# Kernel optimization log

Hardware: AMD Instinct MI355X
Metric: run time of the kernel (lower is better)

## Reference

```python
import jax, jax.numpy as jnp
from jax import lax
import numpy as np

H = 768          # BERT-base hidden size
NLAB = 2         # labelnum
T = NLAB + 2     # CRF tagset incl START/STOP (NCRF++ convention)
START = NLAB     # index 2
STOP = NLAB + 1  # index 3


def setup_inputs() -> dict:
    key = jax.random.key(0)
    ks = jax.random.split(key, 8)
    B, S1 = 64, 513  # S1 = 1 (CLS) + 512 content tokens
    emb = jax.random.normal(ks[0], (B, S1, H), dtype=jnp.float32)
    answer_seq_label = jax.random.randint(ks[1], (B, S1), 0, NLAB)
    IsQA = jax.random.randint(ks[2], (B,), 0, 2)
    fc2_W = jax.random.normal(ks[3], (2, H), dtype=jnp.float32) * 0.02
    fc2_b = jnp.zeros((2,), dtype=jnp.float32)
    crf_W = jax.random.normal(ks[4], (T, H), dtype=jnp.float32) * 0.02
    crf_b = jnp.zeros((T,), dtype=jnp.float32)
    transitions = jax.random.normal(ks[5], (T, T), dtype=jnp.float32) * 0.1
    return {"emb": emb, "answer_seq_label": answer_seq_label, "IsQA": IsQA,
            "fc2_W": fc2_W, "fc2_b": fc2_b, "crf_W": crf_W, "crf_b": crf_b,
            "transitions": transitions}


def _crf_log_partition(feats, trans):
    # feats [B,S,T]; linear-chain forward algorithm (log-sum-exp scan)
    alpha0 = feats[:, 0] + trans[START][None]           # [B,T]
    def step(alpha, feat_t):
        # alpha[b,prev] + trans[prev,cur] -> logsumexp over prev
        new = jax.nn.logsumexp(alpha[:, :, None] + trans[None], axis=1) + feat_t
        return new, None
    alpha, _ = lax.scan(step, alpha0, jnp.swapaxes(feats[:, 1:], 0, 1))
    return jax.nn.logsumexp(alpha + trans[:, STOP][None], axis=1)  # [B]


def _crf_gold_score(feats, tags, trans):
    # feats [B,S,T], tags [B,S]
    emit = jnp.take_along_axis(feats, tags[:, :, None], axis=2)[..., 0].sum(axis=1)
    tr = trans[tags[:, :-1], tags[:, 1:]].sum(axis=1)
    tr = tr + trans[START, tags[:, 0]] + trans[tags[:, -1], STOP]
    return emit + tr


def _crf_viterbi(feats, trans):
    # feats [B,S,T] -> best path [B,S]
    delta0 = feats[:, 0] + trans[START][None]
    def step(delta, feat_t):
        scores = delta[:, :, None] + trans[None]   # [B,prev,cur]
        bp = jnp.argmax(scores, axis=1)            # [B,T]
        return jnp.max(scores, axis=1) + feat_t, bp
    delta, bps = lax.scan(step, delta0, jnp.swapaxes(feats[:, 1:], 0, 1))  # bps [S-1,B,T]
    last_tag = jnp.argmax(delta + trans[:, STOP][None], axis=1)            # [B]
    def back(tag, bp_t):
        prev = jnp.take_along_axis(bp_t, tag[:, None], axis=1)[:, 0]
        return prev, prev
    _, path_prefix = lax.scan(back, last_tag, bps, reverse=True)           # [S-1,B]
    return jnp.concatenate([path_prefix, last_tag[None]], axis=0).T        # [B,S]


def reference(emb, answer_seq_label, IsQA, fc2_W, fc2_b, crf_W, crf_b, transitions):
    # CLS head + cross-entropy
    cls_emb = emb[:, 0]                              # [B,H]
    isqa_logits = cls_emb @ fc2_W.T + fc2_b          # [B,2]
    logp = jax.nn.log_softmax(isqa_logits, axis=-1)
    isqa_loss = -jnp.take_along_axis(logp, IsQA[:, None], axis=1).mean()
    isqa_pred = jnp.argmax(isqa_logits, axis=-1)[:, None]
    # CRF head (dropout = identity in eval); feats [B,S,T]
    feats = jnp.einsum('bsh,th->bst', emb[:, 1:], crf_W) + crf_b
    tags = answer_seq_label[:, 1:]
    Z = _crf_log_partition(feats, transitions)
    gold = _crf_gold_score(feats, tags, transitions)
    crf_loss = jnp.mean(Z - gold)
    crf_pred = _crf_viterbi(feats, transitions)
    return (isqa_pred, crf_pred, isqa_loss, crf_loss, tags, IsQA[:, None])
```

## Files before the change

### kernel.cpp

```cpp
#include <hip/hip_runtime.h>
#include <math.h>

#define B     64
#define S1    513
#define S     512
#define H     768
#define T     4
#define START 2
#define STOP  3

#define OUT_ISQA_PRED 0
#define OUT_CRF_PRED  64
#define OUT_ISQA_LOSS 32832
#define OUT_CRF_LOSS  32833
#define OUT_TAGS      32834
#define OUT_ISQA      65602

#define WS_FEATS  0
#define WS_LOGITS (B*S*T)
#define WS_ZG     (B*S*T + 2*B)
#define WS_CNT    (B*S*T + 3*B)
#define WS_FEATST 131280

template<int CTRL>
__device__ __forceinline__ float dppf(float x) {
    int v = __builtin_amdgcn_update_dpp(__builtin_bit_cast(int, x),
                                        __builtin_bit_cast(int, x),
                                        CTRL, 0xF, 0xF, false);
    return __builtin_bit_cast(float, v);
}
template<int CTRL>
__device__ __forceinline__ int dppi(int x) {
    return __builtin_amdgcn_update_dpp(x, x, CTRL, 0xF, 0xF, false);
}

__device__ __forceinline__ float lse4(float x0, float x1, float x2, float x3) {
    float m = fmaxf(fmaxf(x0, x1), fmaxf(x2, x3));
    return m + __logf(__expf(x0 - m) + __expf(x1 - m) +
                      __expf(x2 - m) + __expf(x3 - m));
}

__device__ __forceinline__ float wred(float a) {
    a += dppf<0xB1>(a); a += dppf<0x4E>(a);
    a += __shfl_xor(a, 4); a += __shfl_xor(a, 8);
    a += __shfl_xor(a, 16); a += __shfl_xor(a, 32);
    return a;
}

__global__ __launch_bounds__(256) void feats_kernel(
    const float* __restrict__ emb,
    const float* __restrict__ crf_W, const float* __restrict__ crf_b,
    float* __restrict__ ws)
{
    if (blockIdx.x == 0 && threadIdx.x == 0)
        ((int*)ws)[WS_CNT] = 0;

    const int tid  = threadIdx.x;
    const int lane = tid & 63;
    const int wid  = blockIdx.x * 4 + (tid >> 6);

    const float4* __restrict__ W4 = (const float4*)crf_W;
    float4 wr[4][3];
    #pragma unroll
    for (int o = 0; o < 4; ++o)
        #pragma unroll
        for (int k = 0; k < 3; ++k)
            wr[o][k] = W4[o * 192 + lane + 64 * k];
    const float cb0 = crf_b[0], cb1 = crf_b[1], cb2 = crf_b[2], cb3 = crf_b[3];

    float* __restrict__ fN = ws + WS_FEATS;
    float* __restrict__ fT = ws + WS_FEATST;

    #pragma unroll
    for (int i = 0; i < 8; ++i) {
        const int row = wid + 4096 * i;
        const int b   = row >> 9;
        const int s   = (row & 511) + 1;
        const float4* __restrict__ src4 =
            (const float4*)emb + (size_t)(b * S1 + s) * (H / 4);

        float a0 = 0.f, a1 = 0.f, a2 = 0.f, a3 = 0.f;
        #pragma unroll
        for (int k = 0; k < 3; ++k) {
            const float4 e = src4[lane + 64 * k];
            a0 += e.x * wr[0][k].x + e.y * wr[0][k].y + e.z * wr[0][k].z + e.w * wr[0][k].w;
            a1 += e.x * wr[1][k].x + e.y * wr[1][k].y + e.z * wr[1][k].z + e.w * wr[1][k].w;
            a2 += e.x * wr[2][k].x + e.y * wr[2][k].y + e.z * wr[2][k].z + e.w * wr[2][k].w;
            a3 += e.x * wr[3][k].x + e.y * wr[3][k].y + e.z * wr[3][k].z + e.w * wr[3][k].w;
        }
        a0 = wred(a0); a1 = wred(a1); a2 = wred(a2); a3 = wred(a3);

        if (lane == 0) {
            const float v0 = a0 + cb0, v1 = a1 + cb1, v2 = a2 + cb2, v3 = a3 + cb3;
            ((float4*)fN)[b * S + (s - 1)] = make_float4(v0, v1, v2, v3);
            const int tb = b * 4 * S + (s - 1);
            fT[tb + 0 * S] = v0;
            fT[tb + 1 * S] = v1;
            fT[tb + 2 * S] = v2;
            fT[tb + 3 * S] = v3;
        }
    }
}

__device__ __forceinline__ unsigned int vstep(
    float& d, float fv,
    float tc0, float tc1, float tc2, float tc3, int sh8j)
{
    const float d0 = dppf<0x00>(d), d1 = dppf<0x55>(d);
    const float d2 = dppf<0xAA>(d), d3 = dppf<0xFF>(d);
    const float y0 = d0 + tc0, y1 = d1 + tc1;
    const float y2 = d2 + tc2, y3 = d3 + tc3;
    const float m01 = fmaxf(y0, y1), m23 = fmaxf(y2, y3);
    const int   i01 = (y1 > y0) ? 1 : 0;
    const int   i23 = (y3 > y2) ? 3 : 2;
    const int   bi  = (m23 > m01) ? i23 : i01;
    d = fmaxf(m01, m23) + fv;
    unsigned int mb = (unsigned int)bi << sh8j;
    unsigned int t1 = mb | (unsigned int)dppi<0xB1>((int)mb);
    return t1 | (unsigned int)dppi<0x4E>((int)t1);
}

__global__ __launch_bounds__(256) void crf_kernel(
    const int* __restrict__ ans, const int* __restrict__ isqa,
    const float* __restrict__ emb,
    const float* __restrict__ fc2_W, const float* __restrict__ fc2_b,
    const float* __restrict__ trans,
    float* __restrict__ ws, float* __restrict__ out)
{
    __shared__ float smemf[10784];
    __shared__ int isLast;
    const int tid = threadIdx.x;
    const int blk = blockIdx.x;

    if (blk < 64) {
        const int b = blk;
        float* sf  = smemf;
        float* C   = smemf + 2048;
        float* red = smemf + 3072;

        float tr[16];
        #pragma unroll
        for (int i = 0; i < 16; ++i) tr[i] = trans[i];

        {
            float4* sf4 = (float4*)sf;
            const float4* src4 = (const float4*)(ws + WS_FEATS) + b * 512;
            sf4[tid] = src4[tid];
            sf4[tid + 256] = src4[tid + 256];
        }

        if (tid < 128) {
            const int wv   = tid >> 6;
            const int lane = tid & 63;
            const float4* e4 = (const float4*)emb + (size_t)b * S1 * (H / 4);
            const float4* w4 = (const float4*)fc2_W + wv * 192;
            float acc = 0.f;
            #pragma unroll
            for (int k = 0; k < 3; ++k) {
                const float4 e = e4[lane + 64 * k];
                const float4 w = w4[lane + 64 * k];
                acc += e.x * w.x + e.y * w.y + e.z * w.z + e.w * w.w;
            }
            acc = wred(acc);
            if (lane == 0) {
                ws[WS_LOGITS + 2 * b + wv] = acc + fc2_b[wv];
                __threadfence();
            }
        }
        __syncthreads();

        float g = 0.f;
        #pragma unroll
        for (int u = 0; u < 2; ++u) {
            const int t   = 2 * tid + u;
            const int tag = ans[b * S1 + 1 + t];
            out[OUT_TAGS + b * S + t] = (float)tag;
            g += sf[t * 4 + tag];
            g += (t == 0) ? tr[START * 4 + tag] : tr[ans[b * S1 + t] * 4 + tag];
            if (t == S - 1) g += tr[tag * 4 + STOP];
        }
        #pragma unroll
        for (int m = 32; m; m >>= 1) g += __shfl_xor(g, m);
        if ((tid & 63) == 0) red[tid >> 6] = g;

        const int c  = tid >> 2;
        const int jr = tid & 3;
        const int t0 = c ? 8 * c : 1;
        float rl[4];
        #pragma unroll
        for (int i = 0; i < 4; ++i) rl[i] = tr[jr * 4 + i] + sf[t0 * 4 + i];
        for (int t = t0 + 1; t <= 8 * c + 7; ++t) {
            const float f0 = sf[t*4+0], f1 = sf[t*4+1], f2 = sf[t*4+2], f3 = sf[t*4+3];
            float nr[4];
            #pragma unroll
            for (int i = 0; i < 4; ++i)
                nr[i] = lse4(rl[0] + tr[0*4+i], rl[1] + tr[1*4+i],
                             rl[2] + tr[2*4+i], rl[3] + tr[3*4+i]);
            rl[0] = nr[0] + f0; rl[1] = nr[1] + f1;
            rl[2] = nr[2] + f2; rl[3] = nr[3] + f3;
        }
        ((float4*)C)[c * 4 + jr] = make_float4(rl[0], rl[1], rl[2], rl[3]);
        __syncthreads();

        for (int d = 1; d <= 32; d <<= 1) {
            const int cs = (c >= d) ? (c - d) : c;
            float4 ar = ((float4*)C)[cs * 4 + jr];
            float4 b0 = ((float4*)C)[c * 4 + 0];
            float4 b1 = ((float4*)C)[c * 4 + 1];
            float4 b2 = ((float4*)C)[c * 4 + 2];
            float4 b3 = ((float4*)C)[c * 4 + 3];
            __syncthreads();
            if (c >= d) {
                float4 nr;
                nr.x = lse4(ar.x + b0.x, ar.y + b1.x, ar.z + b2.x, ar.w + b3.x);
                nr.y = lse4(ar.x + b0.y, ar.y + b1.y, ar.z + b2.y, ar.w + b3.y);
                nr.z = lse4(ar.x + b0.z, ar.y + b1.z, ar.z + b2.z, ar.w + b3.z);
                nr.w = lse4(ar.x + b0.w, ar.y + b1.w, ar.z + b2.w, ar.w + b3.w);
                ((float4*)C)[c * 4 + jr] = nr;
            }
            __syncthreads();
        }

        if (tid == 0) {
            const float gold = red[0] + red[1] + red[2] + red[3];
            float a0k[4];
            #pragma unroll
            for (int k = 0; k < 4; ++k) a0k[k] = sf[k] + tr[START * 4 + k];
            const float* P = C + 63 * 16;
            float aN[4];
            #pragma unroll
            for (int i = 0; i < 4; ++i)
                aN[i] = lse4(a0k[0] + P[0*4+i], a0k[1] + P[1*4+i],
                             a0k[2] + P[2*4+i], a0k[3] + P[3*4+i]);
            const float Z = lse4(aN[0] + tr[0*4+STOP], aN[1] + tr[1*4+STOP],
                                 aN[2] + tr[2*4+STOP], aN[3] + tr[3*4+STOP]);
            ws[WS_ZG + b] = Z - gold;
            out[OUT_ISQA + b] = (float)isqa[b];
            __threadfence();
            const int old = atomicAdd((int*)ws + WS_CNT, 1);
            isLast = (old == 63);
        }
        __syncthreads();

        if (isLast && tid < 64) {
            __threadfence();
            const float zg = ws[WS_ZG + tid];
            const float l0 = ws[WS_LOGITS + tid * 2 + 0];
            const float l1 = ws[WS_LOGITS + tid * 2 + 1];
            const float m  = fmaxf(l0, l1);
            const float lse = m + __logf(__expf(l0 - m) + __expf(l1 - m));
            const int   y   = isqa[tid];
            const float li  = lse - (y ? l1 : l0);
            float s1 = zg, s2 = li;
            #pragma unroll
            for (int d = 32; d; d >>= 1) {
                s1 += __shfl_xor(s1, d);
                s2 += __shfl_xor(s2, d);
            }
            out[OUT_ISQA_PRED + tid] = (l1 > l0) ? 1.0f : 0.0f;
            if (tid == 0) {
                out[OUT_CRF_LOSS]  = s1 * (1.0f / 64.0f);
                out[OUT_ISQA_LOSS] = s2 * (1.0f / 64.0f);
            }
        }
    } else {
        const int bv = blk - 64;
        float* sfT = smemf;
        unsigned int* bpw = (unsigned int*)(smemf + 8208);
        {
            float4* d4 = (float4*)sfT;
            const float4* s4 = (const float4*)(ws + WS_FEATST) + bv * 4 * 512;
            #pragma unroll
            for (int n = 0; n < 8; ++n) d4[tid + 256 * n] = s4[tid + 256 * n];
        }
        if (tid < 4) ((float4*)(sfT + 8192))[tid & 3] =
            make_float4(0.f, 0.f, 0.f, 0.f);
        __syncthreads();

        const int w    = tid >> 6;
        const int lane = tid & 63;
        const int j    = lane & 3;
        const int b    = bv * 4 + w;
        const int sh8j = 8 * j;

        const float tc0 = trans[0*4+j], tc1 = trans[1*4+j];
        const float tc2 = trans[2*4+j], tc3 = trans[3*4+j];
        const float tSj = trans[START*4+j];
        const float tjs = trans[j*4 + STOP];

        const float4* colT4 = (const float4*)(sfT + w * 2048 + j * 512);
        uint4* bpq = (uint4*)(bpw + w * 512);

        float4 A  = colT4[0];
        float4 Bq = colT4[1];
        float4 B2 = colT4[2];
        float d = A.x + tSj;
        {
            const unsigned int W1 = vstep(d, A.y, tc0, tc1, tc2, tc3, sh8j);
            const unsigned int W2 = vstep(d, A.z, tc0, tc1, tc2, tc3, sh8j);
            const unsigned int W3 = vstep(d, A.w, tc0, tc1, tc2, tc3, sh8j);
            if (lane == 0) bpq[0] = make_uint4(0x03020100u, W1, W2, W3);
        }
        for (int g = 1; g < 128; ++g) {
            const float4 Cq = colT4[g + 2];
            const unsigned int W0 = vstep(d, Bq.x, tc0, tc1, tc2, tc3, sh8j);
            const unsigned int W1 = vstep(d, Bq.y, tc0, tc1, tc2, tc3, sh8j);
            const unsigned int W2 = vstep(d, Bq.z, tc0, tc1, tc2, tc3, sh8j);
            const unsigned int W3 = vstep(d, Bq.w, tc0, tc1, tc2, tc3, sh8j);
            if (lane == 0) bpq[g] = make_uint4(W0, W1, W2, W3);
            Bq = B2; B2 = Cq;
        }

        const float vj = d + tjs;
        const float z0 = dppf<0x00>(vj), z1 = dppf<0x55>(vj);
        const float z2 = dppf<0xAA>(vj), z3 = dppf<0xFF>(vj);
        float m01 = z0; unsigned int i01 = 0;
        if (z1 > m01) { m01 = z1; i01 = 1; }
        float m23 = z2; unsigned int i23 = 2;
        if (z3 > m23) { m23 = z3; i23 = 3; }
        const unsigned int lt = (m23 > m01) ? i23 : i01;

        __syncthreads();

        const uint4 wv0 = bpq[lane * 2 + 0];
        const uint4 wv1 = bpq[lane * 2 + 1];
        unsigned int wk[8] = {wv0.x, wv0.y, wv0.z, wv0.w, wv1.x, wv1.y, wv1.z, wv1.w};
        unsigned int G = wk[7];
        #pragma unroll
        for (int k = 6; k >= 0; --k)
            G = __builtin_amdgcn_perm(0u, wk[k], G);
        unsigned int Sm = G;
        #pragma unroll
        for (int dd = 1; dd < 64; dd <<= 1) {
            const int srcl = lane + dd;
            const unsigned int oth = __shfl(Sm, (srcl < 64) ? srcl : 63);
            if (srcl < 64) Sm = __builtin_amdgcn_perm(0u, Sm, oth);
        }
        unsigned int emap = __shfl(Sm, (lane < 63) ? lane + 1 : 63);
        if (lane == 63) emap = 0x03020100u;
        unsigned int cur = (emap >> (8 * lt)) & 3u;

        float tg[8];
        tg[7] = (float)cur;
        #pragma unroll
        for (int k = 7; k >= 1; --k) {
            cur = (wk[k] >> (8 * cur)) & 3u;
            tg[k - 1] = (float)cur;
        }
        float4* op = (float4*)(out + OUT_CRF_PRED + b * S + lane * 8);
        op[0] = make_float4(tg[0], tg[1], tg[2], tg[3]);
        op[1] = make_float4(tg[4], tg[5], tg[6], tg[7]);
    }
}

extern "C" void kernel_launch(void* const* d_in, const int* in_sizes, int n_in,
                              void* d_out, int out_size, void* d_ws, size_t ws_size,
                              hipStream_t stream)
{
    const float* emb    = (const float*)d_in[0];
    const int*   ans    = (const int*)d_in[1];
    const int*   isqa   = (const int*)d_in[2];
    const float* fc2_W  = (const float*)d_in[3];
    const float* fc2_b  = (const float*)d_in[4];
    const float* crf_W  = (const float*)d_in[5];
    const float* crf_b  = (const float*)d_in[6];
    const float* trans  = (const float*)d_in[7];
    float* out = (float*)d_out;
    float* ws  = (float*)d_ws;

    feats_kernel<<<1024, 256, 0, stream>>>(emb, crf_W, crf_b, ws);
    crf_kernel<<<80, 256, 0, stream>>>(ans, isqa, emb, fc2_W, fc2_b, trans, ws, out);
}
```

Baseline: 195.1 us.

## Fuse feats and CRF kernels into one cooperative launch with grid sync

Merges the emission-feature projection and the CRF/Viterbi stage into a single cooperative kernel of 512 blocks separated by a grid-wide sync, removing one launch and the gap between kernels. Each wave now handles two rows per iteration so more loads are in flight. Viterbi backpointers are kept in per-lane registers through predicated selects instead of going through shared memory and a block barrier. Costs are a grid sync, fewer blocks for the memory-bound projection, and extra register pressure and compare work in the Viterbi loop.

```diff
diff --git a/kernel.cpp b/kernel.cpp
--- a/kernel.cpp
+++ b/kernel.cpp
@@ -1,5 +1,8 @@
 #include <hip/hip_runtime.h>
+#include <hip/hip_cooperative_groups.h>
 #include <math.h>
+
+namespace cg = cooperative_groups;
 
 #define B     64
 #define S1    513
@@ -47,59 +50,8 @@
     return a;
 }
 
-__global__ __launch_bounds__(256) void feats_kernel(
-    const float* __restrict__ emb,
-    const float* __restrict__ crf_W, const float* __restrict__ crf_b,
-    float* __restrict__ ws)
-{
-    if (blockIdx.x == 0 && threadIdx.x == 0)
-        ((int*)ws)[WS_CNT] = 0;
-
-    const int tid  = threadIdx.x;
-    const int lane = tid & 63;
-    const int wid  = blockIdx.x * 4 + (tid >> 6);
-
-    const float4* __restrict__ W4 = (const float4*)crf_W;
-    float4 wr[4][3];
-    #pragma unroll
-    for (int o = 0; o < 4; ++o)
-        #pragma unroll
-        for (int k = 0; k < 3; ++k)
-            wr[o][k] = W4[o * 192 + lane + 64 * k];
-    const float cb0 = crf_b[0], cb1 = crf_b[1], cb2 = crf_b[2], cb3 = crf_b[3];
-
-    float* __restrict__ fN = ws + WS_FEATS;
-    float* __restrict__ fT = ws + WS_FEATST;
-
-    #pragma unroll
-    for (int i = 0; i < 8; ++i) {
-        const int row = wid + 4096 * i;
-        const int b   = row >> 9;
-        const int s   = (row & 511) + 1;
-        const float4* __restrict__ src4 =
-            (const float4*)emb + (size_t)(b * S1 + s) * (H / 4);
-
-        float a0 = 0.f, a1 = 0.f, a2 = 0.f, a3 = 0.f;
-        #pragma unroll
-        for (int k = 0; k < 3; ++k) {
-            const float4 e = src4[lane + 64 * k];
-            a0 += e.x * wr[0][k].x + e.y * wr[0][k].y + e.z * wr[0][k].z + e.w * wr[0][k].w;
-            a1 += e.x * wr[1][k].x + e.y * wr[1][k].y + e.z * wr[1][k].z + e.w * wr[1][k].w;
-            a2 += e.x * wr[2][k].x + e.y * wr[2][k].y + e.z * wr[2][k].z + e.w * wr[2][k].w;
-            a3 += e.x * wr[3][k].x + e.y * wr[3][k].y + e.z * wr[3][k].z + e.w * wr[3][k].w;
-        }
-        a0 = wred(a0); a1 = wred(a1); a2 = wred(a2); a3 = wred(a3);
-
-        if (lane == 0) {
-            const float v0 = a0 + cb0, v1 = a1 + cb1, v2 = a2 + cb2, v3 = a3 + cb3;
-            ((float4*)fN)[b * S + (s - 1)] = make_float4(v0, v1, v2, v3);
-            const int tb = b * 4 * S + (s - 1);
-            fT[tb + 0 * S] = v0;
-            fT[tb + 1 * S] = v1;
-            fT[tb + 2 * S] = v2;
-            fT[tb + 3 * S] = v3;
-        }
-    }
+__device__ __forceinline__ float dot4(float4 e, float4 w) {
+    return e.x * w.x + e.y * w.y + e.z * w.z + e.w * w.w;
 }
 
 __device__ __forceinline__ unsigned int vstep(
@@ -120,17 +72,81 @@
     return t1 | (unsigned int)dppi<0x4E>((int)t1);
 }
 
-__global__ __launch_bounds__(256) void crf_kernel(
+__global__ __launch_bounds__(256) void fused_kernel(
     const int* __restrict__ ans, const int* __restrict__ isqa,
     const float* __restrict__ emb,
     const float* __restrict__ fc2_W, const float* __restrict__ fc2_b,
+    const float* __restrict__ crf_W, const float* __restrict__ crf_b,
     const float* __restrict__ trans,
     float* __restrict__ ws, float* __restrict__ out)
 {
-    __shared__ float smemf[10784];
+    __shared__ float smemf[8208];
     __shared__ int isLast;
-    const int tid = threadIdx.x;
-    const int blk = blockIdx.x;
+    const int tid  = threadIdx.x;
+    const int lane = tid & 63;
+    const int blk  = blockIdx.x;
+
+    if (blk == 0 && tid == 0) ((int*)ws)[WS_CNT] = 0;
+    {
+        const int wid = blk * 4 + (tid >> 6);
+        const float4* __restrict__ W4 = (const float4*)crf_W;
+        float4 wr[4][3];
+        #pragma unroll
+        for (int o = 0; o < 4; ++o)
+            #pragma unroll
+            for (int k = 0; k < 3; ++k)
+                wr[o][k] = W4[o * 192 + lane + 64 * k];
+        const float cb0 = crf_b[0], cb1 = crf_b[1], cb2 = crf_b[2], cb3 = crf_b[3];
+        float* __restrict__ fN = ws + WS_FEATS;
+        float* __restrict__ fT = ws + WS_FEATST;
+
+        #pragma unroll 2
+        for (int i = 0; i < 16; i += 2) {
+            const int r0 = wid + 2048 * i;
+            const int r1 = wid + 2048 * (i + 1);
+            const int b0 = r0 >> 9, s0 = (r0 & 511) + 1;
+            const int b1 = r1 >> 9, s1 = (r1 & 511) + 1;
+            const float4* __restrict__ p0 =
+                (const float4*)emb + (size_t)(b0 * S1 + s0) * (H / 4);
+            const float4* __restrict__ p1 =
+                (const float4*)emb + (size_t)(b1 * S1 + s1) * (H / 4);
+            float4 e0[3], e1[3];
+            #pragma unroll
+            for (int k = 0; k < 3; ++k) e0[k] = p0[lane + 64 * k];
+            #pragma unroll
+            for (int k = 0; k < 3; ++k) e1[k] = p1[lane + 64 * k];
+
+            float a00 = 0.f, a01 = 0.f, a02 = 0.f, a03 = 0.f;
+            float a10 = 0.f, a11 = 0.f, a12 = 0.f, a13 = 0.f;
+            #pragma unroll
+            for (int k = 0; k < 3; ++k) {
+                a00 += dot4(e0[k], wr[0][k]); a01 += dot4(e0[k], wr[1][k]);
+                a02 += dot4(e0[k], wr[2][k]); a03 += dot4(e0[k], wr[3][k]);
+                a10 += dot4(e1[k], wr[0][k]); a11 += dot4(e1[k], wr[1][k]);
+                a12 += dot4(e1[k], wr[2][k]); a13 += dot4(e1[k], wr[3][k]);
+            }
+            a00 = wred(a00); a01 = wred(a01); a02 = wred(a02); a03 = wred(a03);
+            a10 = wred(a10); a11 = wred(a11); a12 = wred(a12); a13 = wred(a13);
+
+            if (lane == 0) {
+                const float v0 = a00 + cb0, v1 = a01 + cb1;
+                const float v2 = a02 + cb2, v3 = a03 + cb3;
+                ((float4*)fN)[b0 * S + (s0 - 1)] = make_float4(v0, v1, v2, v3);
+                const int tb0 = b0 * 4 * S + (s0 - 1);
+                fT[tb0 + 0 * S] = v0; fT[tb0 + 1 * S] = v1;
+                fT[tb0 + 2 * S] = v2; fT[tb0 + 3 * S] = v3;
+                const float u0 = a10 + cb0, u1 = a11 + cb1;
+                const float u2 = a12 + cb2, u3 = a13 + cb3;
+                ((float4*)fN)[b1 * S + (s1 - 1)] = make_float4(u0, u1, u2, u3);
+                const int tb1 = b1 * 4 * S + (s1 - 1);
+                fT[tb1 + 0 * S] = u0; fT[tb1 + 1 * S] = u1;
+                fT[tb1 + 2 * S] = u2; fT[tb1 + 3 * S] = u3;
+            }
+        }
+    }
+
+    __threadfence();
+    cg::this_grid().sync();
 
     if (blk < 64) {
         const int b = blk;
@@ -150,8 +166,7 @@
         }
 
         if (tid < 128) {
-            const int wv   = tid >> 6;
-            const int lane = tid & 63;
+            const int wv = tid >> 6;
             const float4* e4 = (const float4*)emb + (size_t)b * S1 * (H / 4);
             const float4* w4 = (const float4*)fc2_W + wv * 192;
             float acc = 0.f;
@@ -159,7 +174,7 @@
             for (int k = 0; k < 3; ++k) {
                 const float4 e = e4[lane + 64 * k];
                 const float4 w = w4[lane + 64 * k];
-                acc += e.x * w.x + e.y * w.y + e.z * w.z + e.w * w.w;
+                acc += dot4(e, w);
             }
             acc = wred(acc);
             if (lane == 0) {
@@ -263,10 +278,9 @@
                 out[OUT_ISQA_LOSS] = s2 * (1.0f / 64.0f);
             }
         }
-    } else {
+    } else if (blk < 80) {
         const int bv = blk - 64;
         float* sfT = smemf;
-        unsigned int* bpw = (unsigned int*)(smemf + 8208);
         {
             float4* d4 = (float4*)sfT;
             const float4* s4 = (const float4*)(ws + WS_FEATST) + bv * 4 * 512;
@@ -278,7 +292,6 @@
         __syncthreads();
 
         const int w    = tid >> 6;
-        const int lane = tid & 63;
         const int j    = lane & 3;
         const int b    = bv * 4 + w;
         const int sh8j = 8 * j;
@@ -289,8 +302,8 @@
         const float tjs = trans[j*4 + STOP];
 
         const float4* colT4 = (const float4*)(sfT + w * 2048 + j * 512);
-        uint4* bpq = (uint4*)(bpw + w * 512);
-
+
+        unsigned int wk[8] = {0, 0, 0, 0, 0, 0, 0, 0};
         float4 A  = colT4[0];
         float4 Bq = colT4[1];
         float4 B2 = colT4[2];
@@ -299,7 +312,7 @@
             const unsigned int W1 = vstep(d, A.y, tc0, tc1, tc2, tc3, sh8j);
             const unsigned int W2 = vstep(d, A.z, tc0, tc1, tc2, tc3, sh8j);
             const unsigned int W3 = vstep(d, A.w, tc0, tc1, tc2, tc3, sh8j);
-            if (lane == 0) bpq[0] = make_uint4(0x03020100u, W1, W2, W3);
+            if (lane == 0) { wk[0] = 0x03020100u; wk[1] = W1; wk[2] = W2; wk[3] = W3; }
         }
         for (int g = 1; g < 128; ++g) {
             const float4 Cq = colT4[g + 2];
@@ -307,7 +320,8 @@
             const unsigned int W1 = vstep(d, Bq.y, tc0, tc1, tc2, tc3, sh8j);
             const unsigned int W2 = vstep(d, Bq.z, tc0, tc1, tc2, tc3, sh8j);
             const unsigned int W3 = vstep(d, Bq.w, tc0, tc1, tc2, tc3, sh8j);
-            if (lane == 0) bpq[g] = make_uint4(W0, W1, W2, W3);
+            if (g == 2 * lane)     { wk[0] = W0; wk[1] = W1; wk[2] = W2; wk[3] = W3; }
+            if (g == 2 * lane + 1) { wk[4] = W0; wk[5] = W1; wk[6] = W2; wk[7] = W3; }
             Bq = B2; B2 = Cq;
         }
 
@@ -320,11 +334,6 @@
         if (z3 > m23) { m23 = z3; i23 = 3; }
         const unsigned int lt = (m23 > m01) ? i23 : i01;
 
-        __syncthreads();
-
-        const uint4 wv0 = bpq[lane * 2 + 0];
-        const uint4 wv1 = bpq[lane * 2 + 1];
-        unsigned int wk[8] = {wv0.x, wv0.y, wv0.z, wv0.w, wv1.x, wv1.y, wv1.z, wv1.w};
         unsigned int G = wk[7];
         #pragma unroll
         for (int k = 6; k >= 0; --k)
@@ -357,9 +366,9 @@
                               void* d_out, int out_size, void* d_ws, size_t ws_size,
                               hipStream_t stream)
 {
-    const float* emb    = (const float*)d_in[0];
     const int*   ans    = (const int*)d_in[1];
     const int*   isqa   = (const int*)d_in[2];
+    const float* emb    = (const float*)d_in[0];
     const float* fc2_W  = (const float*)d_in[3];
     const float* fc2_b  = (const float*)d_in[4];
     const float* crf_W  = (const float*)d_in[5];
@@ -368,6 +377,9 @@
     float* out = (float*)d_out;
     float* ws  = (float*)d_ws;
 
-    feats_kernel<<<1024, 256, 0, stream>>>(emb, crf_W, crf_b, ws);
-    crf_kernel<<<80, 256, 0, stream>>>(ans, isqa, emb, fc2_W, fc2_b, trans, ws, out);
-}
+    void* args[] = {(void*)&ans, (void*)&isqa, (void*)&emb,
+                    (void*)&fc2_W, (void*)&fc2_b, (void*)&crf_W, (void*)&crf_b,
+                    (void*)&trans, (void*)&ws, (void*)&out};
+    hipLaunchCooperativeKernel((void*)fused_kernel, dim3(512), dim3(256),
+                               args, 0, stream);
+}
```

New measurement: 312.0 us. 59.9% more time.

## Compute CRF emission feats with one thread per row instead of one wave per row

Applied to the files above, without the earlier changes.

The feats kernel now assigns each token row to a single thread that loops over the full hidden dimension, reading emb and the broadcast crf_W directly. This removes the cross-lane wave reductions and the 8-row loop per wave, and the launch shrinks to 512 blocks of 64 threads. In exchange, lanes in a wave read rows spaced 3 KB apart, so the loads are no longer coalesced. The kernel also runs far fewer waves, which reduces latency hiding on a bandwidth-bound read.

```diff
diff --git a/kernel.cpp b/kernel.cpp
--- a/kernel.cpp
+++ b/kernel.cpp
@@ -47,7 +47,11 @@
     return a;
 }
 
-__global__ __launch_bounds__(256) void feats_kernel(
+__device__ __forceinline__ float dot4(float4 e, float4 w) {
+    return e.x * w.x + e.y * w.y + e.z * w.z + e.w * w.w;
+}
+
+__global__ __launch_bounds__(64) void feats_kernel(
     const float* __restrict__ emb,
     const float* __restrict__ crf_W, const float* __restrict__ crf_b,
     float* __restrict__ ws)
@@ -55,51 +59,42 @@
     if (blockIdx.x == 0 && threadIdx.x == 0)
         ((int*)ws)[WS_CNT] = 0;
 
-    const int tid  = threadIdx.x;
-    const int lane = tid & 63;
-    const int wid  = blockIdx.x * 4 + (tid >> 6);
-
+    const int lane = threadIdx.x;
+    const int r    = blockIdx.x * 64 + lane;
+    const int b    = r >> 9;
+    const int s    = (r & 511) + 1;
+
+    const float4* __restrict__ src4 =
+        (const float4*)emb + (size_t)(b * S1 + s) * (H / 4);
     const float4* __restrict__ W4 = (const float4*)crf_W;
-    float4 wr[4][3];
-    #pragma unroll
-    for (int o = 0; o < 4; ++o)
-        #pragma unroll
-        for (int k = 0; k < 3; ++k)
-            wr[o][k] = W4[o * 192 + lane + 64 * k];
-    const float cb0 = crf_b[0], cb1 = crf_b[1], cb2 = crf_b[2], cb3 = crf_b[3];
+
+    float a0 = 0.f, a1 = 0.f, a2 = 0.f, a3 = 0.f;
+    #pragma unroll 8
+    for (int k = 0; k < 192; ++k) {
+        const float4 e  = src4[k];
+        const float4 w0 = W4[0 * 192 + k];
+        const float4 w1 = W4[1 * 192 + k];
+        const float4 w2 = W4[2 * 192 + k];
+        const float4 w3 = W4[3 * 192 + k];
+        a0 += dot4(e, w0);
+        a1 += dot4(e, w1);
+        a2 += dot4(e, w2);
+        a3 += dot4(e, w3);
+    }
+
+    const float v0 = a0 + crf_b[0];
+    const float v1 = a1 + crf_b[1];
+    const float v2 = a2 + crf_b[2];
+    const float v3 = a3 + crf_b[3];
 
     float* __restrict__ fN = ws + WS_FEATS;
     float* __restrict__ fT = ws + WS_FEATST;
-
-    #pragma unroll
-    for (int i = 0; i < 8; ++i) {
-        const int row = wid + 4096 * i;
-        const int b   = row >> 9;
-        const int s   = (row & 511) + 1;
-        const float4* __restrict__ src4 =
-            (const float4*)emb + (size_t)(b * S1 + s) * (H / 4);
-
-        float a0 = 0.f, a1 = 0.f, a2 = 0.f, a3 = 0.f;
-        #pragma unroll
-        for (int k = 0; k < 3; ++k) {
-            const float4 e = src4[lane + 64 * k];
-            a0 += e.x * wr[0][k].x + e.y * wr[0][k].y + e.z * wr[0][k].z + e.w * wr[0][k].w;
-            a1 += e.x * wr[1][k].x + e.y * wr[1][k].y + e.z * wr[1][k].z + e.w * wr[1][k].w;
-            a2 += e.x * wr[2][k].x + e.y * wr[2][k].y + e.z * wr[2][k].z + e.w * wr[2][k].w;
-            a3 += e.x * wr[3][k].x + e.y * wr[3][k].y + e.z * wr[3][k].z + e.w * wr[3][k].w;
-        }
-        a0 = wred(a0); a1 = wred(a1); a2 = wred(a2); a3 = wred(a3);
-
-        if (lane == 0) {
-            const float v0 = a0 + cb0, v1 = a1 + cb1, v2 = a2 + cb2, v3 = a3 + cb3;
-            ((float4*)fN)[b * S + (s - 1)] = make_float4(v0, v1, v2, v3);
-            const int tb = b * 4 * S + (s - 1);
-            fT[tb + 0 * S] = v0;
-            fT[tb + 1 * S] = v1;
-            fT[tb + 2 * S] = v2;
-            fT[tb + 3 * S] = v3;
-        }
-    }
+    ((float4*)fN)[b * S + (s - 1)] = make_float4(v0, v1, v2, v3);
+    const int tb = b * 4 * S + (s - 1);
+    fT[tb + 0 * S] = v0;
+    fT[tb + 1 * S] = v1;
+    fT[tb + 2 * S] = v2;
+    fT[tb + 3 * S] = v3;
 }
 
 __device__ __forceinline__ unsigned int vstep(
@@ -159,7 +154,7 @@
             for (int k = 0; k < 3; ++k) {
                 const float4 e = e4[lane + 64 * k];
                 const float4 w = w4[lane + 64 * k];
-                acc += e.x * w.x + e.y * w.y + e.z * w.z + e.w * w.w;
+                acc += dot4(e, w);
             }
             acc = wred(acc);
             if (lane == 0) {
@@ -368,6 +363,6 @@
     float* out = (float*)d_out;
     float* ws  = (float*)d_ws;
 
-    feats_kernel<<<1024, 256, 0, stream>>>(emb, crf_W, crf_b, ws);
+    feats_kernel<<<512, 64, 0, stream>>>(emb, crf_W, crf_b, ws);
     crf_kernel<<<80, 256, 0, stream>>>(ans, isqa, emb, fc2_W, fc2_b, trans, ws, out);
 }
```

After: 224.3 us. +15.0%, slower.

## Stage embedding rows through double-buffered LDS in CRF feature projection kernel

Applied to the files above, without the earlier changes.

Rewrites the feature projection kernel so each block stages chunks of 8 embedding rows into a double-buffered shared-memory tile, prefetching the next chunk while the current one is reduced. Each 32-lane group handles one row with 6 float4 columns per lane instead of a full wave per row, which changes the reduction to shuffle-based. The aim is to overlap global loads with compute and raise occupancy via launch bounds. The cost is more LDS, a barrier per chunk, and larger register weight tiles. The launch grid must match the new rows-per-block mapping (32 rows per block versus 32 per block before), which appears consistent.

```diff
diff --git a/kernel.cpp b/kernel.cpp
--- a/kernel.cpp
+++ b/kernel.cpp
@@ -22,6 +22,10 @@
 #define WS_CNT    (B*S*T + 3*B)
 #define WS_FEATST 131280
 
+#define FRB  8
+#define FNC  4
+#define FRS  193
+
 template<int CTRL>
 __device__ __forceinline__ float dppf(float x) {
     int v = __builtin_amdgcn_update_dpp(__builtin_bit_cast(int, x),
@@ -47,59 +51,94 @@
     return a;
 }
 
-__global__ __launch_bounds__(256) void feats_kernel(
+__device__ __forceinline__ float dot4(float4 e, float4 w) {
+    return e.x * w.x + e.y * w.y + e.z * w.z + e.w * w.w;
+}
+
+__global__ __launch_bounds__(256, 3) void feats_kernel(
     const float* __restrict__ emb,
     const float* __restrict__ crf_W, const float* __restrict__ crf_b,
     float* __restrict__ ws)
 {
-    if (blockIdx.x == 0 && threadIdx.x == 0)
-        ((int*)ws)[WS_CNT] = 0;
-
-    const int tid  = threadIdx.x;
-    const int lane = tid & 63;
-    const int wid  = blockIdx.x * 4 + (tid >> 6);
+    __shared__ float4 buf[2][FRB * FRS];
+
+    const int tid = threadIdx.x;
+    const int blk = blockIdx.x;
+    if (blk == 0 && tid == 0) ((int*)ws)[WS_CNT] = 0;
+
+    const int q  = tid & 31;
+    const int rb = tid >> 5;
 
     const float4* __restrict__ W4 = (const float4*)crf_W;
-    float4 wr[4][3];
+    float4 wq[4][6];
     #pragma unroll
     for (int o = 0; o < 4; ++o)
         #pragma unroll
-        for (int k = 0; k < 3; ++k)
-            wr[o][k] = W4[o * 192 + lane + 64 * k];
+        for (int k = 0; k < 6; ++k)
+            wq[o][k] = W4[o * 192 + q + 32 * k];
     const float cb0 = crf_b[0], cb1 = crf_b[1], cb2 = crf_b[2], cb3 = crf_b[3];
 
+    const float4* __restrict__ emb4 = (const float4*)emb;
     float* __restrict__ fN = ws + WS_FEATS;
     float* __restrict__ fT = ws + WS_FEATST;
-
-    #pragma unroll
-    for (int i = 0; i < 8; ++i) {
-        const int row = wid + 4096 * i;
-        const int b   = row >> 9;
-        const int s   = (row & 511) + 1;
-        const float4* __restrict__ src4 =
-            (const float4*)emb + (size_t)(b * S1 + s) * (H / 4);
-
+    const int row0 = blk * (FRB * FNC);
+
+    #define STAGE(c, sb)                                                      \
+    {                                                                         \
+        _Pragma("unroll")                                                     \
+        for (int n = 0; n < 6; ++n) {                                         \
+            const int idx = tid + 256 * n;                                    \
+            const int r   = idx / 192;                                        \
+            const int k4  = idx - r * 192;                                    \
+            const int row = row0 + (c) * FRB + r;                             \
+            const int bb  = row >> 9;                                         \
+            const int ss  = (row & 511) + 1;                                  \
+            buf[sb][r * FRS + k4] =                                           \
+                emb4[(size_t)(bb * S1 + ss) * (H / 4) + k4];                  \
+        }                                                                     \
+    }
+
+    STAGE(0, 0);
+    __syncthreads();
+
+    int pb = 0;
+    for (int c = 0; c < FNC; ++c) {
+        if (c + 1 < FNC) STAGE(c + 1, pb ^ 1);
+
+        const float4* __restrict__ rowp = &buf[pb][rb * FRS];
         float a0 = 0.f, a1 = 0.f, a2 = 0.f, a3 = 0.f;
         #pragma unroll
-        for (int k = 0; k < 3; ++k) {
-            const float4 e = src4[lane + 64 * k];
-            a0 += e.x * wr[0][k].x + e.y * wr[0][k].y + e.z * wr[0][k].z + e.w * wr[0][k].w;
-            a1 += e.x * wr[1][k].x + e.y * wr[1][k].y + e.z * wr[1][k].z + e.w * wr[1][k].w;
-            a2 += e.x * wr[2][k].x + e.y * wr[2][k].y + e.z * wr[2][k].z + e.w * wr[2][k].w;
-            a3 += e.x * wr[3][k].x + e.y * wr[3][k].y + e.z * wr[3][k].z + e.w * wr[3][k].w;
-        }
-        a0 = wred(a0); a1 = wred(a1); a2 = wred(a2); a3 = wred(a3);
-
-        if (lane == 0) {
-            const float v0 = a0 + cb0, v1 = a1 + cb1, v2 = a2 + cb2, v3 = a3 + cb3;
-            ((float4*)fN)[b * S + (s - 1)] = make_float4(v0, v1, v2, v3);
-            const int tb = b * 4 * S + (s - 1);
+        for (int k = 0; k < 6; ++k) {
+            const float4 e = rowp[q + 32 * k];
+            a0 += dot4(e, wq[0][k]);
+            a1 += dot4(e, wq[1][k]);
+            a2 += dot4(e, wq[2][k]);
+            a3 += dot4(e, wq[3][k]);
+        }
+        #pragma unroll
+        for (int d = 1; d <= 16; d <<= 1) {
+            a0 += __shfl_xor(a0, d);
+            a1 += __shfl_xor(a1, d);
+            a2 += __shfl_xor(a2, d);
+            a3 += __shfl_xor(a3, d);
+        }
+        if (q == 0) {
+            const int row = row0 + c * FRB + rb;
+            const int bb  = row >> 9;
+            const int ss  = (row & 511) + 1;
+            const float v0 = a0 + cb0, v1 = a1 + cb1;
+            const float v2 = a2 + cb2, v3 = a3 + cb3;
+            ((float4*)fN)[bb * S + (ss - 1)] = make_float4(v0, v1, v2, v3);
+            const int tb = bb * 4 * S + (ss - 1);
             fT[tb + 0 * S] = v0;
             fT[tb + 1 * S] = v1;
             fT[tb + 2 * S] = v2;
             fT[tb + 3 * S] = v3;
         }
+        __syncthreads();
+        pb ^= 1;
     }
+    #undef STAGE
 }
 
 __device__ __forceinline__ unsigned int vstep(
@@ -159,7 +198,7 @@
             for (int k = 0; k < 3; ++k) {
                 const float4 e = e4[lane + 64 * k];
                 const float4 w = w4[lane + 64 * k];
-                acc += e.x * w.x + e.y * w.y + e.z * w.z + e.w * w.w;
+                acc += dot4(e, w);
             }
             acc = wred(acc);
             if (lane == 0) {
```

Result: no change. 198.7 us (+1.9%).
